# Kernel tuning notes

Measured on AMD Instinct MI355X. Metric: run time of the kernel, lower is better.

The kernel has to match this reference:

```python
import jax, jax.numpy as jnp
import numpy as np

N_NODES = 100000
N_EDGES = 1600000
D_FEAT = 48


def sage_conv(x, src, dst, Wl, Wr, b):
    # mean aggregation of neighbor messages x[src] at dst (PyG source_to_target)
    msg_sum = jax.ops.segment_sum(x[src], dst, num_segments=N_NODES)  # [N, d]
    cnt = jax.ops.segment_sum(jnp.ones((src.shape[0],), x.dtype), dst,
                              num_segments=N_NODES)  # [N]
    mean = msg_sum / jnp.maximum(cnt, 1.0)[:, None]
    # out = lin_l(mean neighbors) + lin_r(self); bias only on lin_l (PyG default)
    return mean @ Wl + b + x @ Wr


def setup_inputs() -> dict:
    key = jax.random.key(0)
    ks = jax.random.split(key, 8)
    x = jax.random.normal(ks[0], (N_NODES, D_FEAT), jnp.float32)
    edge_index = jax.random.randint(ks[1], (2, N_EDGES), 0, N_NODES, jnp.int64)
    def w(k, fi, fo):
        return jax.random.normal(k, (fi, fo), jnp.float32) / np.sqrt(fi)
    return {
        "x": x,
        "edge_index": edge_index,
        "W1l": w(ks[2], D_FEAT, 32), "W1r": w(ks[3], D_FEAT, 32),
        "b1": jnp.zeros((32,), jnp.float32),
        "W2l": w(ks[4], 32, 16), "W2r": w(ks[5], 32, 16),
        "b2": jnp.zeros((16,), jnp.float32),
        "Wlin": w(ks[6], 16, 2), "blin": jnp.zeros((2,), jnp.float32),
    }


def reference(x, edge_index, W1l, W1r, b1, W2l, W2r, b2, Wlin, blin):
    src, dst = edge_index[0], edge_index[1]
    h = jax.nn.relu(sage_conv(x, src, dst, W1l, W1r, b1))
    h = jax.nn.relu(sage_conv(h, src, dst, W2l, W2r, b2))
    return h @ Wlin + blin  # [N, 2] logits
```

## Files before the change

### kernel.cpp

```cpp
#include <hip/hip_runtime.h>
#include <hip/hip_bf16.h>


constexpr int NN  = 100000;
constexpr int NE  = 1600000;
constexpr int NLN = 391;
constexpr int NB  = 391;
constexpr int CAP = 4608;
constexpr int SEG = CAP + 3 * 256;
constexpr int T1  = 2048;
constexpr int NB1 = (NE + T1 - 1) / T1;

__device__ __forceinline__ float bl(unsigned u) { return __uint_as_float(u << 16); }
__device__ __forceinline__ float bh(unsigned u) { return __uint_as_float(u & 0xffff0000u); }
__device__ __forceinline__ unsigned f2b(float x) {
    unsigned u = __float_as_uint(x);
    return (u + 0x7fffu + ((u >> 16) & 1u)) >> 16;
}
__device__ __forceinline__ unsigned pack2(float a, float b) {
    return f2b(a) | (f2b(b) << 16);
}

__device__ __forceinline__ int wave_incl_scan(int v, int lane) {
#pragma unroll
    for (int d = 1; d < 64; d <<= 1) {
        int t = __shfl_up(v, d, 64);
        if (lane >= d) v += t;
    }
    return v;
}

__global__ __launch_bounds__(256) void k1_kernel(
    const float* __restrict__ X,
    const float* __restrict__ Wl,
    const float* __restrict__ Wr,
    const int*   __restrict__ ei,
    int* __restrict__ bsize, unsigned* __restrict__ bbuf,
    __hip_bfloat16* __restrict__ P, __hip_bfloat16* __restrict__ R)
{
    __shared__ float sW1[48 * 32];
    __shared__ int hist[NB], base[NB];
    __shared__ int s_any;

    if (blockIdx.x < 2 * NLN) {
        const bool isP = blockIdx.x < NLN;
        const float* W = isP ? Wl : Wr;
        __hip_bfloat16* O = isP ? P : R;
        for (int i = threadIdx.x; i < 48 * 32; i += 256)
            sW1[i] = W[i];
        __syncthreads();
        int n = (blockIdx.x - (isP ? 0 : NLN)) * 256 + threadIdx.x;
        if (n > NN) return;
        if (n == NN) {
            if (isP) {
                uint4 z = make_uint4(0, 0, 0, 0);
                uint4* pp = reinterpret_cast<uint4*>(P + (size_t)NN * 32);
#pragma unroll
                for (int i = 0; i < 4; ++i) pp[i] = z;
            }
            return;
        }
        float xr[48];
        const float4* xp = reinterpret_cast<const float4*>(X + (size_t)n * 48);
#pragma unroll
        for (int i = 0; i < 12; ++i) {
            float4 u = xp[i];
            xr[i*4+0] = u.x; xr[i*4+1] = u.y; xr[i*4+2] = u.z; xr[i*4+3] = u.w;
        }
        float acc[32];
#pragma unroll
        for (int j = 0; j < 32; ++j) acc[j] = 0.f;
#pragma unroll
        for (int k = 0; k < 48; ++k) {
            float xk = xr[k];
#pragma unroll
            for (int j = 0; j < 32; ++j)
                acc[j] += xk * sW1[k * 32 + j];
        }
        uint4* op = reinterpret_cast<uint4*>(O + (size_t)n * 32);
#pragma unroll
        for (int i = 0; i < 4; ++i) {
            uint4 u;
            u.x = pack2(acc[i*8+0], acc[i*8+1]); u.y = pack2(acc[i*8+2], acc[i*8+3]);
            u.z = pack2(acc[i*8+4], acc[i*8+5]); u.w = pack2(acc[i*8+6], acc[i*8+7]);
            op[i] = u;
        }
    } else {
        if (threadIdx.x == 0) s_any = 0;
        for (int i = threadIdx.x; i < NB; i += 256) hist[i] = 0;
        __syncthreads();
        int dv = 0;
        for (int i = threadIdx.x; i < 2048; i += 256) dv |= ei[2 * i + 1];
        if (dv != 0) atomicOr(&s_any, 1);
        __syncthreads();
        const bool i64 = (s_any == 0);
        const int e0 = (blockIdx.x - 2 * NLN) * T1;

        auto sweep = [&](auto&& f) {
            if (i64) {
                const int4* sp = reinterpret_cast<const int4*>(ei) + (e0 >> 1);
                const int4* dp = reinterpret_cast<const int4*>(ei) + ((NE + e0) >> 1);
#pragma unroll
                for (int it = 0; it < 4; ++it) {
                    int p = it * 256 + threadIdx.x;
                    int e = e0 + 2 * p;
                    if (e + 2 <= NE) {
                        int4 s4 = sp[p], d4 = dp[p];
                        f(s4.x, d4.x);
                        f(s4.z, d4.z);
                    } else {
                        for (int e2 = e; e2 < NE && e2 < e + 2; ++e2)
                            f(ei[(size_t)e2 << 1], ei[(size_t)(NE + e2) << 1]);
                    }
                }
            } else {
                const int4* sp = reinterpret_cast<const int4*>(ei) + (e0 >> 2);
                const int4* dp = reinterpret_cast<const int4*>(ei) + ((NE + e0) >> 2);
#pragma unroll
                for (int it = 0; it < 2; ++it) {
                    int q = it * 256 + threadIdx.x;
                    int e = e0 + 4 * q;
                    if (e + 4 <= NE) {
                        int4 s4 = sp[q], d4 = dp[q];
                        f(s4.x, d4.x);
                        f(s4.y, d4.y);
                        f(s4.z, d4.z);
                        f(s4.w, d4.w);
                    } else {
                        for (int e2 = e; e2 < NE && e2 < e + 4; ++e2)
                            f(ei[e2], ei[NE + e2]);
                    }
                }
            }
        };

        sweep([&](int s, int d) {
            if ((unsigned)s < (unsigned)NN && (unsigned)d < (unsigned)NN)
                atomicAdd(&hist[d >> 8], 1);
        });
        __syncthreads();
        for (int b = threadIdx.x; b < NB; b += 256) {
            int h = hist[b];
            base[b] = h ? atomicAdd(&bsize[b], h) : 0;
        }
        __syncthreads();
        sweep([&](int s, int d) {
            if ((unsigned)s < (unsigned)NN && (unsigned)d < (unsigned)NN) {
                int bk = d >> 8;
                int pos = atomicAdd(&base[bk], 1);
                if (pos < CAP)
                    bbuf[(size_t)bk * CAP + pos] =
                        ((unsigned)s << 8) | (unsigned)(d & 255);
            }
        });
    }
}

__global__ __launch_bounds__(1024) void kg1_kernel(
    const int* __restrict__ bsize, const unsigned* __restrict__ bbuf,
    const __hip_bfloat16* __restrict__ p1,
    const __hip_bfloat16* __restrict__ r1,
    const float* __restrict__ b1,
    const float* __restrict__ W2l,
    const float* __restrict__ W2r,
    int* __restrict__ csr_g,
    int* __restrict__ deg_g,
    int* __restrict__ rows_g,
    __hip_bfloat16* __restrict__ P2,
    __hip_bfloat16* __restrict__ R2)
{
    __shared__ alignas(16) int csr[SEG + 8];
    __shared__ int ldeg[256], lcur[256], ws[4];
    __shared__ float sW2l[32 * 16], sW2r[32 * 16], sb1[32];
    __shared__ float shh[32 * 257];

    int t = threadIdx.x, b = blockIdx.x;
    if (t < 512) { sW2l[t] = W2l[t]; sW2r[t] = W2r[t]; }
    else if (t < 544) sb1[t - 512] = b1[t - 512];
    if (t < 256) ldeg[t] = 0;
    __syncthreads();

    int S = min(bsize[b], CAP);
    const unsigned* bp = bbuf + (size_t)b * CAP;
    for (int i = t; i < S; i += 1024)
        atomicAdd(&ldeg[bp[i] & 255u], 1);
    __syncthreads();

    int v = 0, pv = 0, incl = 0, excl = 0;
    if (t < 256) {
        v  = ldeg[t];
        pv = (v + 3) & ~3;
        incl = wave_incl_scan(pv, t & 63);
        if ((t & 63) == 63) ws[t >> 6] = incl;
    }
    __syncthreads();
    if (t < 256) {
        int off = 0, wid = t >> 6;
#pragma unroll
        for (int w = 0; w < 3; ++w)
            if (wid > w) off += ws[w];
        excl = off + incl - pv;
        lcur[t] = excl;
        int node = (b << 8) + t;
        if (node < NN) {
            deg_g[node] = v;
            rows_g[node] = b * SEG + excl;
        }
    }
    __syncthreads();
    for (int i = t; i < S; i += 1024) {
        unsigned pk = bp[i];
        int pos = atomicAdd(&lcur[pk & 255u], 1);
        csr[pos] = (int)(pk >> 8);
    }
    if (t < 256)
        for (int p = excl + v; p < excl + pv; ++p)
            csr[p] = NN;
    __syncthreads();

    for (int p = t; p < SEG; p += 1024)
        csr_g[b * SEG + p] = csr[p];

    int loc = t >> 2, c = t & 3;
    int n = (b << 8) + loc;
    if (n < NN) {
        int dn = ldeg[loc];
        int start = lcur[loc] - dn;
        int pv4 = ((dn + 3) & ~3) >> 2;
        const uint4* prow = reinterpret_cast<const uint4*>(p1);
        const int4* cp4 = reinterpret_cast<const int4*>(csr + start);
        uint4 r = reinterpret_cast<const uint4*>(r1)[(size_t)n * 4 + c];
        float acc[8];
#pragma unroll
        for (int j = 0; j < 8; ++j) acc[j] = 0.f;
        int k = 0;
        int4 sA = cp4[0];
        int4 sB = cp4[1];
        for (; k + 1 < pv4; k += 2) {
            int4 nA = cp4[k + 2];
            int4 nB = cp4[k + 3];
            uint4 a = prow[(size_t)sA.x * 4 + c];
            uint4 bq = prow[(size_t)sA.y * 4 + c];
            uint4 d = prow[(size_t)sA.z * 4 + c];
            uint4 e = prow[(size_t)sA.w * 4 + c];
            uint4 f = prow[(size_t)sB.x * 4 + c];
            uint4 g = prow[(size_t)sB.y * 4 + c];
            uint4 hq = prow[(size_t)sB.z * 4 + c];
            uint4 m = prow[(size_t)sB.w * 4 + c];
            acc[0] += bl(a.x) + bl(bq.x) + bl(d.x) + bl(e.x)
                    + bl(f.x) + bl(g.x) + bl(hq.x) + bl(m.x);
            acc[1] += bh(a.x) + bh(bq.x) + bh(d.x) + bh(e.x)
                    + bh(f.x) + bh(g.x) + bh(hq.x) + bh(m.x);
            acc[2] += bl(a.y) + bl(bq.y) + bl(d.y) + bl(e.y)
                    + bl(f.y) + bl(g.y) + bl(hq.y) + bl(m.y);
            acc[3] += bh(a.y) + bh(bq.y) + bh(d.y) + bh(e.y)
                    + bh(f.y) + bh(g.y) + bh(hq.y) + bh(m.y);
            acc[4] += bl(a.z) + bl(bq.z) + bl(d.z) + bl(e.z)
                    + bl(f.z) + bl(g.z) + bl(hq.z) + bl(m.z);
            acc[5] += bh(a.z) + bh(bq.z) + bh(d.z) + bh(e.z)
                    + bh(f.z) + bh(g.z) + bh(hq.z) + bh(m.z);
            acc[6] += bl(a.w) + bl(bq.w) + bl(d.w) + bl(e.w)
                    + bl(f.w) + bl(g.w) + bl(hq.w) + bl(m.w);
            acc[7] += bh(a.w) + bh(bq.w) + bh(d.w) + bh(e.w)
                    + bh(f.w) + bh(g.w) + bh(hq.w) + bh(m.w);
            sA = nA; sB = nB;
        }
        if (k < pv4) {
            uint4 a = prow[(size_t)sA.x * 4 + c];
            uint4 bq = prow[(size_t)sA.y * 4 + c];
            uint4 d = prow[(size_t)sA.z * 4 + c];
            uint4 e = prow[(size_t)sA.w * 4 + c];
            acc[0] += bl(a.x) + bl(bq.x) + bl(d.x) + bl(e.x);
            acc[1] += bh(a.x) + bh(bq.x) + bh(d.x) + bh(e.x);
            acc[2] += bl(a.y) + bl(bq.y) + bl(d.y) + bl(e.y);
            acc[3] += bh(a.y) + bh(bq.y) + bh(d.y) + bh(e.y);
            acc[4] += bl(a.z) + bl(bq.z) + bl(d.z) + bl(e.z);
            acc[5] += bh(a.z) + bh(bq.z) + bh(d.z) + bh(e.z);
            acc[6] += bl(a.w) + bl(bq.w) + bl(d.w) + bl(e.w);
            acc[7] += bh(a.w) + bh(bq.w) + bh(d.w) + bh(e.w);
        }
        float inv = 1.0f / fmaxf((float)dn, 1.0f);
        float rr[8] = { bl(r.x), bh(r.x), bl(r.y), bh(r.y),
                        bl(r.z), bh(r.z), bl(r.w), bh(r.w) };
#pragma unroll
        for (int j = 0; j < 8; ++j)
            shh[(c * 8 + j) * 257 + loc] =
                fmaxf(acc[j] * inv + rr[j] + sb1[c * 8 + j], 0.f);
    } else if (n == NN) {
        uint2 z = make_uint2(0, 0);
        reinterpret_cast<uint2*>(P2)[(size_t)NN * 4 + c] = z;
        reinterpret_cast<uint2*>(R2)[(size_t)NN * 4 + c] = z;
    }
    __syncthreads();

    if (n < NN) {
        float accp[4], accr[4];
#pragma unroll
        for (int j = 0; j < 4; ++j) { accp[j] = 0.f; accr[j] = 0.f; }
#pragma unroll
        for (int k2i = 0; k2i < 32; ++k2i) {
            float hk = shh[k2i * 257 + loc];
#pragma unroll
            for (int j = 0; j < 4; ++j) {
                accp[j] += hk * sW2l[k2i * 16 + c * 4 + j];
                accr[j] += hk * sW2r[k2i * 16 + c * 4 + j];
            }
        }
        uint2 up, ur;
        up.x = pack2(accp[0], accp[1]); up.y = pack2(accp[2], accp[3]);
        ur.x = pack2(accr[0], accr[1]); ur.y = pack2(accr[2], accr[3]);
        reinterpret_cast<uint2*>(P2)[(size_t)n * 4 + c] = up;
        reinterpret_cast<uint2*>(R2)[(size_t)n * 4 + c] = ur;
    }
}

__global__ __launch_bounds__(256) void gather2_kernel(
    const int* __restrict__ rowstart, const int* __restrict__ deg,
    const int* __restrict__ csr_src,
    const __hip_bfloat16* __restrict__ P2,
    const __hip_bfloat16* __restrict__ R2,
    const float* __restrict__ b2,
    const float* __restrict__ Wlin,
    const float* __restrict__ blin,
    float* __restrict__ out)
{
    __shared__ float sb[16], sW[32], sbl[2];
    if (threadIdx.x < 16) sb[threadIdx.x] = b2[threadIdx.x];
    else if (threadIdx.x < 48) sW[threadIdx.x - 16] = Wlin[threadIdx.x - 16];
    else if (threadIdx.x < 50) sbl[threadIdx.x - 48] = blin[threadIdx.x - 48];
    __syncthreads();
    int t = blockIdx.x * 256 + threadIdx.x;
    int n = t >> 2, c = t & 3;
    if (n >= NN) return;
    int start = rowstart[n], dn = deg[n];
    int pv4 = ((dn + 3) & ~3) >> 2;

    const uint2* prow = reinterpret_cast<const uint2*>(P2);
    const int4* cp4 = reinterpret_cast<const int4*>(csr_src + start);
    uint2 r = reinterpret_cast<const uint2*>(R2)[(size_t)n * 4 + c];
    float acc[4];
#pragma unroll
    for (int j = 0; j < 4; ++j) acc[j] = 0.f;
    int k = 0;
    int4 sA = cp4[0];
    int4 sB = cp4[1];
    for (; k + 1 < pv4; k += 2) {
        int4 nA = cp4[k + 2];
        int4 nB = cp4[k + 3];
        uint2 a = prow[(size_t)sA.x * 4 + c];
        uint2 b = prow[(size_t)sA.y * 4 + c];
        uint2 d = prow[(size_t)sA.z * 4 + c];
        uint2 e = prow[(size_t)sA.w * 4 + c];
        uint2 f = prow[(size_t)sB.x * 4 + c];
        uint2 g = prow[(size_t)sB.y * 4 + c];
        uint2 h = prow[(size_t)sB.z * 4 + c];
        uint2 m = prow[(size_t)sB.w * 4 + c];
        acc[0] += bl(a.x) + bl(b.x) + bl(d.x) + bl(e.x)
                + bl(f.x) + bl(g.x) + bl(h.x) + bl(m.x);
        acc[1] += bh(a.x) + bh(b.x) + bh(d.x) + bh(e.x)
                + bh(f.x) + bh(g.x) + bh(h.x) + bh(m.x);
        acc[2] += bl(a.y) + bl(b.y) + bl(d.y) + bl(e.y)
                + bl(f.y) + bl(g.y) + bl(h.y) + bl(m.y);
        acc[3] += bh(a.y) + bh(b.y) + bh(d.y) + bh(e.y)
                + bh(f.y) + bh(g.y) + bh(h.y) + bh(m.y);
        sA = nA; sB = nB;
    }
    if (k < pv4) {
        uint2 a = prow[(size_t)sA.x * 4 + c];
        uint2 b = prow[(size_t)sA.y * 4 + c];
        uint2 d = prow[(size_t)sA.z * 4 + c];
        uint2 e = prow[(size_t)sA.w * 4 + c];
        acc[0] += bl(a.x) + bl(b.x) + bl(d.x) + bl(e.x);
        acc[1] += bh(a.x) + bh(b.x) + bh(d.x) + bh(e.x);
        acc[2] += bl(a.y) + bl(b.y) + bl(d.y) + bl(e.y);
        acc[3] += bh(a.y) + bh(b.y) + bh(d.y) + bh(e.y);
    }
    float inv = 1.0f / fmaxf((float)dn, 1.0f);
    float rr[4] = { bl(r.x), bh(r.x), bl(r.y), bh(r.y) };
    float o0 = 0.f, o1 = 0.f;
#pragma unroll
    for (int j = 0; j < 4; ++j) {
        int kk = c * 4 + j;
        float hv = fmaxf(acc[j] * inv + rr[j] + sb[kk], 0.f);
        o0 += hv * sW[kk * 2];
        o1 += hv * sW[kk * 2 + 1];
    }
    o0 += __shfl_xor(o0, 1, 64);
    o1 += __shfl_xor(o1, 1, 64);
    o0 += __shfl_xor(o0, 2, 64);
    o1 += __shfl_xor(o1, 2, 64);
    if (c == 0)
        reinterpret_cast<float2*>(out)[n] = make_float2(o0 + sbl[0], o1 + sbl[1]);
}

extern "C" void kernel_launch(void* const* d_in, const int* in_sizes, int n_in,
                              void* d_out, int out_size, void* d_ws, size_t ws_size,
                              hipStream_t stream)
{
    const float* x    = (const float*)d_in[0];
    const int*   ei   = (const int*)d_in[1];
    const float* W1l  = (const float*)d_in[2];
    const float* W1r  = (const float*)d_in[3];
    const float* b1   = (const float*)d_in[4];
    const float* W2l  = (const float*)d_in[5];
    const float* W2r  = (const float*)d_in[6];
    const float* b2   = (const float*)d_in[7];
    const float* Wlin = (const float*)d_in[8];
    const float* blin = (const float*)d_in[9];
    float* out = (float*)d_out;

    char* wsb = (char*)d_ws;
    int*      bsize    = (int*)(wsb + 64);
    int*      deg      = (int*)(wsb + 4096);
    int*      rowstart = (int*)(wsb + 404096);
    int*      csr_g    = (int*)(wsb + 804096);
    unsigned* bbuf     = (unsigned*)(wsb + 9300000);
    __hip_bfloat16* p1 = (__hip_bfloat16*)(wsb + 16600000);
    __hip_bfloat16* r1 = (__hip_bfloat16*)(wsb + 23100000);
    __hip_bfloat16* p2 = (__hip_bfloat16*)(wsb + 29600000);
    __hip_bfloat16* r2 = (__hip_bfloat16*)(wsb + 32900000);

    hipMemsetAsync(bsize, 0, NB * sizeof(int), stream);
    k1_kernel<<<2 * NLN + NB1, dim3(256), 0, stream>>>(
        x, W1l, W1r, ei, bsize, bbuf, p1, r1);
    kg1_kernel<<<NB, dim3(1024), 0, stream>>>(
        bsize, bbuf, p1, r1, b1, W2l, W2r, csr_g, deg, rowstart, p2, r2);
    gather2_kernel<<<(NN * 4 + 255) / 256, dim3(256), 0, stream>>>(
        rowstart, deg, csr_g, p2, r2, b2, Wlin, blin, out);
}
```

Measured before the change: 172.0 us.

## Split each dst bucket across two 512-thread blocks in layer-1 gather kernel

The fused layer-1 gather/CSR-build kernel now launches two 512-thread blocks per 256-node bucket, each handling 128 destination nodes. Each block scans the whole bucket's edge list but keeps only edges for its half, builds its own CSR segment (HSEG per block), and writes rowstart offsets relative to that segment. This raises block count from 391 to 782 so more CUs are occupied with smaller LDS footprints. The cost is that every bucket's edge list is read twice, and the workspace offsets are shifted to fit the larger CSR region.

After: 179.5 us. +4.4%, slower.

```diff
diff --git a/kernel.cpp b/kernel.cpp
--- a/kernel.cpp
+++ b/kernel.cpp
@@ -7,7 +7,7 @@
 constexpr int NLN = 391;
 constexpr int NB  = 391;
 constexpr int CAP = 4608;
-constexpr int SEG = CAP + 3 * 256;
+constexpr int HSEG = CAP + 3 * 128;
 constexpr int T1  = 2048;
 constexpr int NB1 = (NE + T1 - 1) / T1;
 
@@ -156,7 +156,7 @@
     }
 }
 
-__global__ __launch_bounds__(1024) void kg1_kernel(
+__global__ __launch_bounds__(512) void kg1_kernel(
     const int* __restrict__ bsize, const unsigned* __restrict__ bbuf,
     const __hip_bfloat16* __restrict__ p1,
     const __hip_bfloat16* __restrict__ r1,
@@ -169,61 +169,70 @@
     __hip_bfloat16* __restrict__ P2,
     __hip_bfloat16* __restrict__ R2)
 {
-    __shared__ alignas(16) int csr[SEG + 8];
-    __shared__ int ldeg[256], lcur[256], ws[4];
+    __shared__ alignas(16) int csr[HSEG + 8];
+    __shared__ int ldeg[128], lcur[128], ws[2];
     __shared__ float sW2l[32 * 16], sW2r[32 * 16], sb1[32];
-    __shared__ float shh[32 * 257];
-
-    int t = threadIdx.x, b = blockIdx.x;
-    if (t < 512) { sW2l[t] = W2l[t]; sW2r[t] = W2r[t]; }
-    else if (t < 544) sb1[t - 512] = b1[t - 512];
-    if (t < 256) ldeg[t] = 0;
+    __shared__ float shh[32 * 129];
+
+    int t = threadIdx.x;
+    int b = blockIdx.x >> 1, h = blockIdx.x & 1;
+    int gseg = (int)blockIdx.x * HSEG;
+
+    sW2l[t] = W2l[t];
+    sW2r[t] = W2r[t];
+    if (t < 32) sb1[t] = b1[t];
+    if (t < 128) ldeg[t] = 0;
     __syncthreads();
 
     int S = min(bsize[b], CAP);
     const unsigned* bp = bbuf + (size_t)b * CAP;
-    for (int i = t; i < S; i += 1024)
-        atomicAdd(&ldeg[bp[i] & 255u], 1);
+    for (int i = t; i < S; i += 512) {
+        unsigned pk = bp[i];
+        int ln = pk & 255u;
+        if ((ln >> 7) == h) atomicAdd(&ldeg[ln & 127], 1);
+    }
     __syncthreads();
 
     int v = 0, pv = 0, incl = 0, excl = 0;
-    if (t < 256) {
+    if (t < 128) {
         v  = ldeg[t];
         pv = (v + 3) & ~3;
         incl = wave_incl_scan(pv, t & 63);
         if ((t & 63) == 63) ws[t >> 6] = incl;
     }
     __syncthreads();
-    if (t < 256) {
-        int off = 0, wid = t >> 6;
-#pragma unroll
-        for (int w = 0; w < 3; ++w)
-            if (wid > w) off += ws[w];
+    if (t < 128) {
+        int off = (t >> 6) ? ws[0] : 0;
         excl = off + incl - pv;
         lcur[t] = excl;
-        int node = (b << 8) + t;
+        int node = (b << 8) + (h << 7) + t;
         if (node < NN) {
             deg_g[node] = v;
-            rows_g[node] = b * SEG + excl;
-        }
-    }
-    __syncthreads();
-    for (int i = t; i < S; i += 1024) {
+            rows_g[node] = gseg + excl;
+        }
+    }
+    __syncthreads();
+    for (int i = t; i < S; i += 512) {
         unsigned pk = bp[i];
-        int pos = atomicAdd(&lcur[pk & 255u], 1);
-        csr[pos] = (int)(pk >> 8);
-    }
-    if (t < 256)
+        int ln = pk & 255u;
+        if ((ln >> 7) == h) {
+            int pos = atomicAdd(&lcur[ln & 127], 1);
+            csr[pos] = (int)(pk >> 8);
+        }
+    }
+    if (t < 128)
         for (int p = excl + v; p < excl + pv; ++p)
             csr[p] = NN;
     __syncthreads();
 
-    for (int p = t; p < SEG; p += 1024)
-        csr_g[b * SEG + p] = csr[p];
+    for (int p = t; p < HSEG; p += 512)
+        csr_g[gseg + p] = csr[p];
 
     int loc = t >> 2, c = t & 3;
-    int n = (b << 8) + loc;
-    if (n < NN) {
+    int n = (b << 8) + (h << 7) + loc;
+    bool valid = n < NN;
+
+    if (valid) {
         int dn = ldeg[loc];
         int start = lcur[loc] - dn;
         int pv4 = ((dn + 3) & ~3) >> 2;
@@ -284,22 +293,17 @@
                         bl(r.z), bh(r.z), bl(r.w), bh(r.w) };
 #pragma unroll
         for (int j = 0; j < 8; ++j)
-            shh[(c * 8 + j) * 257 + loc] =
-                fmaxf(acc[j] * inv + rr[j] + sb1[c * 8 + j], 0.f);
-    } else if (n == NN) {
-        uint2 z = make_uint2(0, 0);
-        reinterpret_cast<uint2*>(P2)[(size_t)NN * 4 + c] = z;
-        reinterpret_cast<uint2*>(R2)[(size_t)NN * 4 + c] = z;
-    }
-    __syncthreads();
-
-    if (n < NN) {
+            shh[(c * 8 + j) * 129 + loc] = fmaxf(acc[j] * inv + rr[j] + sb1[c * 8 + j], 0.f);
+    }
+    __syncthreads();
+
+    if (valid) {
         float accp[4], accr[4];
 #pragma unroll
         for (int j = 0; j < 4; ++j) { accp[j] = 0.f; accr[j] = 0.f; }
 #pragma unroll
         for (int k2i = 0; k2i < 32; ++k2i) {
-            float hk = shh[k2i * 257 + loc];
+            float hk = shh[k2i * 129 + loc];
 #pragma unroll
             for (int j = 0; j < 4; ++j) {
                 accp[j] += hk * sW2l[k2i * 16 + c * 4 + j];
@@ -311,6 +315,10 @@
         ur.x = pack2(accr[0], accr[1]); ur.y = pack2(accr[2], accr[3]);
         reinterpret_cast<uint2*>(P2)[(size_t)n * 4 + c] = up;
         reinterpret_cast<uint2*>(R2)[(size_t)n * 4 + c] = ur;
+    } else if (n == NN) {
+        uint2 z = make_uint2(0, 0);
+        reinterpret_cast<uint2*>(P2)[(size_t)NN * 4 + c] = z;
+        reinterpret_cast<uint2*>(R2)[(size_t)NN * 4 + c] = z;
     }
 }
 
@@ -414,16 +422,16 @@
     int*      deg      = (int*)(wsb + 4096);
     int*      rowstart = (int*)(wsb + 404096);
     int*      csr_g    = (int*)(wsb + 804096);
-    unsigned* bbuf     = (unsigned*)(wsb + 9300000);
-    __hip_bfloat16* p1 = (__hip_bfloat16*)(wsb + 16600000);
-    __hip_bfloat16* r1 = (__hip_bfloat16*)(wsb + 23100000);
-    __hip_bfloat16* p2 = (__hip_bfloat16*)(wsb + 29600000);
-    __hip_bfloat16* r2 = (__hip_bfloat16*)(wsb + 32900000);
+    unsigned* bbuf     = (unsigned*)(wsb + 16500000);
+    __hip_bfloat16* p1 = (__hip_bfloat16*)(wsb + 23800000);
+    __hip_bfloat16* r1 = (__hip_bfloat16*)(wsb + 30300000);
+    __hip_bfloat16* p2 = (__hip_bfloat16*)(wsb + 36800000);
+    __hip_bfloat16* r2 = (__hip_bfloat16*)(wsb + 40100000);
 
     hipMemsetAsync(bsize, 0, NB * sizeof(int), stream);
     k1_kernel<<<2 * NLN + NB1, dim3(256), 0, stream>>>(
         x, W1l, W1r, ei, bsize, bbuf, p1, r1);
-    kg1_kernel<<<NB, dim3(1024), 0, stream>>>(
+    kg1_kernel<<<2 * NB, dim3(512), 0, stream>>>(
         bsize, bbuf, p1, r1, b1, W2l, W2r, csr_g, deg, rowstart, p2, r2);
     gather2_kernel<<<(NN * 4 + 255) / 256, dim3(256), 0, stream>>>(
         rowstart, deg, csr_g, p2, r2, b2, Wlin, blin, out);
```
